# Kernel tuning notes

Hardware: AMD Instinct MI355X
Metric: run time of the kernel (lower is better)

## Reference

```python
import jax, jax.numpy as jnp
import numpy as np

B, LT, LP = 64, 128, 16   # batch, tweet len, topic len
V, H, H2 = 18000, 768, 768


def setup_inputs() -> dict:
    key = jax.random.key(0)
    ks = jax.random.split(key, 16)
    s = 1.0 / np.sqrt(H2)
    u = lambda k, shape, sc: jax.random.uniform(k, shape, jnp.float32, -sc, sc)
    return {
        "tweet": jax.random.randint(ks[0], (B, LT), 0, V, dtype=jnp.int32),
        "topic": jax.random.randint(ks[1], (B, LP), 0, V, dtype=jnp.int32),
        "beta": jnp.ones((LP,), jnp.float32) / LP,
        "emb": jax.random.normal(ks[2], (V, H), jnp.float32),
        "Wih_f": u(ks[3], (3 * H2, H), s), "Whh_f": u(ks[4], (3 * H2, H2), s),
        "bih_f": u(ks[5], (3 * H2,), s), "bhh_f": u(ks[6], (3 * H2,), s),
        "Wih_b": u(ks[7], (3 * H2, H), s), "Whh_b": u(ks[8], (3 * H2, H2), s),
        "bih_b": u(ks[9], (3 * H2,), s), "bhh_b": u(ks[10], (3 * H2,), s),
        "W_bl": u(ks[11], (2 * H2, 2 * H2), 1.0 / np.sqrt(2 * H2)),
        "det_W": u(ks[12], (2, 4 * H2), 1.0 / np.sqrt(4 * H2)),
        "det_b": u(ks[13], (2,), 1.0 / np.sqrt(4 * H2)),
    }


def _gru_dir(x, Wih, Whh, bih, bhh, reverse):
    # x: [T, N, H] (torch GRU is seq-first: axis0 is time)
    xp = jnp.einsum('tnh,gh->tng', x, Wih) + bih  # [T, N, 3*H2]
    if reverse:
        xp = xp[::-1]

    def step(h, xpt):
        g = h @ Whh.T + bhh
        xr, xz, xn = jnp.split(xpt, 3, axis=-1)
        hr, hz, hn = jnp.split(g, 3, axis=-1)
        r = jax.nn.sigmoid(xr + hr)
        z = jax.nn.sigmoid(xz + hz)
        n = jnp.tanh(xn + r * hn)
        hnew = (1.0 - z) * n + z * h
        return hnew, hnew

    h0 = jnp.zeros((x.shape[1], Whh.shape[1]), x.dtype)
    _, hs = jax.lax.scan(step, h0, xp)
    if reverse:
        hs = hs[::-1]
    return hs


def _bigru(ids, emb, Wih_f, Whh_f, bih_f, bhh_f, Wih_b, Whh_b, bih_b, bhh_b):
    x = emb[ids]  # [B, L, H]; recurrence runs over axis0 (faithful to seq-first nn.GRU)
    f = _gru_dir(x, Wih_f, Whh_f, bih_f, bhh_f, False)
    b = _gru_dir(x, Wih_b, Whh_b, bih_b, bhh_b, True)
    return jnp.concatenate([f, b], axis=-1)  # [B, L, 2*H2]


def reference(tweet, topic, beta, emb, Wih_f, Whh_f, bih_f, bhh_f,
              Wih_b, Whh_b, bih_b, bhh_b, W_bl, det_W, det_b):
    # NOTE: original uses self.gru_tweet for BOTH tweet and topic (faithful)
    tw = _bigru(tweet, emb, Wih_f, Whh_f, bih_f, bhh_f, Wih_b, Whh_b, bih_b, bhh_b)
    tp = _bigru(topic, emb, Wih_f, Whh_f, bih_f, bhh_f, Wih_b, Whh_b, bih_b, bhh_b)
    # BiLinear: S[b,t,l] = topic[b,t] @ W @ tweet[b,l]
    S = jnp.einsum('btk,kd,bld->btl', tp, W_bl, tw)
    att = jax.nn.softmax(S, axis=-1)                    # per-(b,t) softmax over tweet positions
    r = jnp.einsum('btl,bld->btd', att, tw)             # [B, LP, 2*H2]
    mean_r = jnp.einsum('btd,t->bd', r[:, :-1], beta[:-1])  # last j skipped (the `continue`)
    R = jnp.concatenate([r[:, -1], mean_r], axis=-1)    # [B, 4*H2]
    out = R @ det_W.T + det_b                           # detect logits (torch softmax call is a no-op bug)
    return out, R
```

## Files before the change

### kernel.cpp

```cpp
#include <hip/hip_runtime.h>
#include <hip/hip_bf16.h>
#include <cstdint>
#include <cstddef>

#define HD 768
#define GD 2304
#define DD 1536

typedef __attribute__((ext_vector_type(8))) short bfrag8;
typedef __attribute__((ext_vector_type(4))) float f32x4;
typedef unsigned short ushort_t;

static constexpr size_t F_XP_TWF = 0;
static constexpr size_t F_XP_TWB = 18874368;
static constexpr size_t F_XP_TPF = 37748736;
static constexpr size_t F_XP_TPB = 40108032;
static constexpr size_t F_TPWHI  = 0;
static constexpr size_t F_TPWLO  = 786432;
static constexpr size_t F_WBLT_HI = 2000000;
static constexpr size_t F_WBLT_LO = 3200000;
static constexpr size_t F_ATT    = 5000000;
static constexpr size_t F_R      = 6000000;
static constexpr size_t F_B      = 42467328;
static constexpr size_t U_XTW_HI  = 0;
static constexpr size_t U_XTW_LO  = 6291456;
static constexpr size_t U_XTP_HI  = 12582912;
static constexpr size_t U_XTP_LO  = 13369344;
static constexpr size_t U_WIHF_HI = 14155776;
static constexpr size_t U_WIHF_LO = 15925248;
static constexpr size_t U_WIHB_HI = 17694720;
static constexpr size_t U_WIHB_LO = 19464192;
static constexpr size_t U_TWHI   = 0;
static constexpr size_t U_TWLO   = 12582912;
static constexpr size_t U_TPHI   = 25165824;
static constexpr size_t U_TPLO   = 26738688;
static constexpr size_t F_WHH    = F_B + 14155776;
static constexpr size_t U_WHHF_HI = 0;
static constexpr size_t U_WHHF_LO = 1769472;
static constexpr size_t U_WHHB_HI = 3538944;
static constexpr size_t U_WHHB_LO = 5308416;
static constexpr size_t F_H      = F_WHH + 3538944;
static constexpr size_t U_HPAIR  = 442368;
static constexpr size_t U_HLO    = 221184;

__device__ __forceinline__ float sigmoidf_(float x) { return 1.f / (1.f + expf(-x)); }
__device__ __forceinline__ ushort_t f2bf(float f) {
  unsigned int u = __builtin_bit_cast(unsigned int, f);
  unsigned int r = (u + 0x7fffu + ((u >> 16) & 1u)) >> 16;
  return (ushort_t)r;
}
__device__ __forceinline__ float bf2f(ushort_t h) {
  unsigned int u = ((unsigned int)h) << 16;
  return __builtin_bit_cast(float, u);
}
__device__ __forceinline__ void glds16(const ushort_t* src, ushort_t* ldsDst) {
  __builtin_amdgcn_global_load_lds((const void*)src, (void*)ldsDst, 16, 0, 0);
}

__global__ void zero_kernel(float* __restrict__ p, int n) {
  int i = blockIdx.x * 256 + threadIdx.x;
  if (i < n) p[i] = 0.f;
}

__global__ __launch_bounds__(256) void gather_split_kernel(
    const int* __restrict__ ids, const float* __restrict__ emb,
    ushort_t* __restrict__ hi, ushort_t* __restrict__ lo, int total4)
{
  int i = blockIdx.x * 256 + threadIdx.x;
  if (i >= total4) return;
  int r = i / 192;
  int c = (i - r * 192) * 4;
  const float4 v = *reinterpret_cast<const float4*>(emb + (size_t)ids[r] * HD + c);
  float vv[4] = {v.x, v.y, v.z, v.w};
  ushort_t h[4], l[4];
#pragma unroll
  for (int e = 0; e < 4; ++e) { h[e] = f2bf(vv[e]); l[e] = f2bf(vv[e] - bf2f(h[e])); }
  size_t base = (size_t)i * 4;
  *reinterpret_cast<uint2*>(hi + base) = make_uint2((unsigned)h[0] | ((unsigned)h[1] << 16), (unsigned)h[2] | ((unsigned)h[3] << 16));
  *reinterpret_cast<uint2*>(lo + base) = make_uint2((unsigned)l[0] | ((unsigned)l[1] << 16), (unsigned)l[2] | ((unsigned)l[3] << 16));
}

__global__ __launch_bounds__(256) void split_w_kernel(
    const float* __restrict__ src, ushort_t* __restrict__ hi,
    ushort_t* __restrict__ lo, int total4)
{
  int i = blockIdx.x * 256 + threadIdx.x;
  if (i >= total4) return;
  const float4 v = *reinterpret_cast<const float4*>(src + (size_t)i * 4);
  float vv[4] = {v.x, v.y, v.z, v.w};
  ushort_t h[4], l[4];
#pragma unroll
  for (int e = 0; e < 4; ++e) { h[e] = f2bf(vv[e]); l[e] = f2bf(vv[e] - bf2f(h[e])); }
  size_t base = (size_t)i * 4;
  *reinterpret_cast<uint2*>(hi + base) = make_uint2((unsigned)h[0] | ((unsigned)h[1] << 16), (unsigned)h[2] | ((unsigned)h[3] << 16));
  *reinterpret_cast<uint2*>(lo + base) = make_uint2((unsigned)l[0] | ((unsigned)l[1] << 16), (unsigned)l[2] | ((unsigned)l[3] << 16));
}

__global__ __launch_bounds__(256) void transp_split_kernel(
    const float* __restrict__ src, ushort_t* __restrict__ hi, ushort_t* __restrict__ lo)
{
  __shared__ float t[32][33];
  const int bx = blockIdx.x, by = blockIdx.y, tid = threadIdx.x;
  const int r = tid >> 3, c4 = (tid & 7) * 4;
  const float4 v = *reinterpret_cast<const float4*>(src + (size_t)(by * 32 + r) * DD + bx * 32 + c4);
  t[r][c4 + 0] = v.x; t[r][c4 + 1] = v.y; t[r][c4 + 2] = v.z; t[r][c4 + 3] = v.w;
  __syncthreads();
  ushort_t h[4], l[4];
#pragma unroll
  for (int j = 0; j < 4; ++j) {
    float o = t[c4 + j][r];
    h[j] = f2bf(o); l[j] = f2bf(o - bf2f(h[j]));
  }
  size_t ob = (size_t)(bx * 32 + r) * DD + by * 32 + c4;
  *reinterpret_cast<uint2*>(hi + ob) = make_uint2((unsigned)h[0] | ((unsigned)h[1] << 16), (unsigned)h[2] | ((unsigned)h[3] << 16));
  *reinterpret_cast<uint2*>(lo + ob) = make_uint2((unsigned)l[0] | ((unsigned)l[1] << 16), (unsigned)l[2] | ((unsigned)l[3] << 16));
}

template<bool SPLIT_OUT>
__global__ __launch_bounds__(256, 3) void mfma_gemm_kernel(
    const ushort_t* __restrict__ Ahi, const ushort_t* __restrict__ Alo,
    const ushort_t* __restrict__ Bhi, const ushort_t* __restrict__ Blo,
    const float* __restrict__ bias, float* __restrict__ outF,
    ushort_t* __restrict__ outHi, ushort_t* __restrict__ outLo,
    const int K, const int N, const int mgc)
{
  __shared__ __align__(16) ushort_t sm[6][4096];
  const int b = blockIdx.x, nb = gridDim.x;
  const int id = (b & 7) * (nb >> 3) + (b >> 3);
  const int cg = id / mgc, mg = id % mgc;
  const size_t mBase = (size_t)mg * 128, nBase = (size_t)cg * 128;
  const int tid = threadIdx.x, lane = tid & 63, w = tid >> 6;
  const int wr = w >> 1, wc = w & 1;
  const int KB = K >> 5;

  const ushort_t* Ah = Ahi + mBase * K;
  const ushort_t* Al = Alo + mBase * K;
  const ushort_t* Bh = Bhi + nBase * K;
  const ushort_t* Bl = Blo + nBase * K;

  f32x4 acc[4][4];
#pragma unroll
  for (int i = 0; i < 4; ++i)
#pragma unroll
    for (int j = 0; j < 4; ++j) acc[i][j] = (f32x4){0.f, 0.f, 0.f, 0.f};

  auto stageF = [&](int buf, int koff) {
    ushort_t* Bt  = sm[buf * 3 + 0];
    ushort_t* At0 = sm[buf * 3 + 1];
    ushort_t* At1 = sm[buf * 3 + 2];
#pragma unroll
    for (int ii = 0; ii < 2; ++ii) {
      int i16 = w * 2 + ii;
      int row = i16 * 16 + (lane >> 2), c16 = lane & 3;
      size_t so = (size_t)row * K + (size_t)(koff + ((c16 ^ (row & 3)) << 3));
      glds16(Bh + so, Bt + i16 * 512);
      glds16(Ah + so, At0 + i16 * 512);
      glds16(Al + so, At1 + i16 * 512);
    }
  };
  auto stageP = [&](int buf, int koff) {
    ushort_t* Bt  = sm[buf * 3 + 0];
    ushort_t* At0 = sm[buf * 3 + 1];
#pragma unroll
    for (int ii = 0; ii < 2; ++ii) {
      int i16 = w * 2 + ii;
      int row = i16 * 16 + (lane >> 2), c16 = lane & 3;
      size_t so = (size_t)row * K + (size_t)(koff + ((c16 ^ (row & 3)) << 3));
      glds16(Bl + so, Bt + i16 * 512);
      glds16(Ah + so, At0 + i16 * 512);
    }
  };
  const int kch = (lane >> 4) << 4;

  auto compute = [&](int buf, bool both) {
    const char* Bt  = reinterpret_cast<const char*>(sm[buf * 3 + 0]);
    const char* At0 = reinterpret_cast<const char*>(sm[buf * 3 + 1]);
    const char* At1 = reinterpret_cast<const char*>(sm[buf * 3 + 2]);
    bfrag8 bF[4], aF[4];
#pragma unroll
    for (int j = 0; j < 4; ++j) {
      int row = wc * 64 + j * 16 + (lane & 15);
      bF[j] = *reinterpret_cast<const bfrag8*>(Bt + row * 64 + (kch ^ ((row & 3) << 4)));
    }
#pragma unroll
    for (int i = 0; i < 4; ++i) {
      int row = wr * 64 + i * 16 + (lane & 15);
      aF[i] = *reinterpret_cast<const bfrag8*>(At0 + row * 64 + (kch ^ ((row & 3) << 4)));
    }
#pragma unroll
    for (int i = 0; i < 4; ++i)
#pragma unroll
      for (int j = 0; j < 4; ++j)
        acc[i][j] = __builtin_amdgcn_mfma_f32_16x16x32_bf16(aF[i], bF[j], acc[i][j], 0, 0, 0);
    if (both) {
#pragma unroll
      for (int i = 0; i < 4; ++i) {
        int row = wr * 64 + i * 16 + (lane & 15);
        aF[i] = *reinterpret_cast<const bfrag8*>(At1 + row * 64 + (kch ^ ((row & 3) << 4)));
      }
#pragma unroll
      for (int i = 0; i < 4; ++i)
#pragma unroll
        for (int j = 0; j < 4; ++j)
          acc[i][j] = __builtin_amdgcn_mfma_f32_16x16x32_bf16(aF[i], bF[j], acc[i][j], 0, 0, 0);
    }
  };

  stageF(0, 0);
  __syncthreads();
  for (int kb = 0; kb < KB; ++kb) {
    if (kb < KB - 1) stageF((kb + 1) & 1, (kb + 1) * 32);
    else             stageP(0, 0);
    compute(kb & 1, true);
    __syncthreads();
  }
  for (int kb = 0; kb < KB; ++kb) {
    if (kb < KB - 1) stageP((kb + 1) & 1, (kb + 1) * 32);
    compute(kb & 1, false);
    __syncthreads();
  }

#pragma unroll
  for (int i = 0; i < 4; ++i)
#pragma unroll
    for (int j = 0; j < 4; ++j) {
      int col = (int)nBase + wc * 64 + j * 16 + (lane & 15);
#pragma unroll
      for (int p = 0; p < 4; ++p) {
        size_t row = mBase + wr * 64 + i * 16 + ((lane >> 4) << 2) + p;
        if constexpr (SPLIT_OUT) {
          float v = acc[i][j][p];
          ushort_t hh = f2bf(v);
          outHi[row * N + col] = hh;
          outLo[row * N + col] = f2bf(v - bf2f(hh));
        } else {
          outF[row * N + col] = acc[i][j][p] + bias[col];
        }
      }
    }
}

__global__ __launch_bounds__(256) void gru3_kernel(
    const ushort_t* __restrict__ WfHi, const ushort_t* __restrict__ WfLo,
    const ushort_t* __restrict__ WbHi, const ushort_t* __restrict__ WbLo,
    const float* __restrict__ bhhF, const float* __restrict__ bhhB,
    const float* __restrict__ xpTwf, const float* __restrict__ xpTwb,
    const float* __restrict__ xpTpf, const float* __restrict__ xpTpb,
    const ushort_t* __restrict__ Hc, ushort_t* __restrict__ Hn,
    ushort_t* __restrict__ TWhi, ushort_t* __restrict__ TWlo,
    ushort_t* __restrict__ TPhi, ushort_t* __restrict__ TPlo, const int s)
{
  __shared__ __align__(16) ushort_t sm[2][16][512];
  const int bid = blockIdx.x;
  const int xcd = bid & 7, kk = bid >> 3;
  const bool isTweet = (kk < 24);
  const int sl = isTweet ? (kk >> 2) : (kk - 24);
  const int rg = isTweet ? (kk & 3) : 0;
  const int slice = xcd * 6 + sl;
  const int cg = slice >> 1, dir = slice & 1;
  const int j0 = cg * 32;
  const int Mfrags = isTweet ? 2 : 1;
  const int baseR = dir * 144 + (isTweet ? rg * 32 : 128);
  const ushort_t* __restrict__ Whi = dir ? WbHi : WfHi;
  const ushort_t* __restrict__ Wlo = dir ? WbLo : WfLo;
  const float* __restrict__ bhh = dir ? bhhB : bhhF;
  const int tid = threadIdx.x, lane = tid & 63, w = tid >> 6;
  const ushort_t* HcHi = Hc;
  const ushort_t* HcLo = Hc + U_HLO;

  const int mf = isTweet ? (w & 1) : 0;
  const int ch = isTweet ? (w >> 1) : w;
  const bool doCompute = isTweet || (w < 2);

  auto stage = [&](int buf, int kb) {
    const int r16 = lane & 15, k8 = (lane >> 4) << 3;
#pragma unroll
    for (int i = 0; i < 4; ++i) {
      const int slot = w * 4 + i;
      if (slot < 4) {
        const int m = slot >> 1, p = slot & 1;
        if (m < Mfrags) {
          const ushort_t* src = (p ? HcLo : HcHi) +
              (size_t)(baseR + m * 16 + r16) * HD + kb * 32 + k8;
          glds16(src, &sm[buf][slot][0]);
        }
      } else {
        const int idx = slot - 4;
        const int p = idx & 1, c2 = (idx >> 1) & 1, g = idx >> 2;
        const ushort_t* W = p ? Wlo : Whi;
        const ushort_t* src = W +
            (size_t)(g * HD + j0 + c2 * 16 + r16) * HD + kb * 32 + k8;
        glds16(src, &sm[buf][slot][0]);
      }
    }
  };

  f32x4 acc[3];
#pragma unroll
  for (int g = 0; g < 3; ++g) acc[g] = (f32x4){0.f, 0.f, 0.f, 0.f};

  auto computeT = [&](int buf) {
    if (!doCompute) return;
    const char* base = reinterpret_cast<const char*>(&sm[buf][0][0]);
    const int aoff = mf * 2;
    bfrag8 Ah = *reinterpret_cast<const bfrag8*>(base + (aoff + 0) * 1024 + lane * 16);
    bfrag8 Al = *reinterpret_cast<const bfrag8*>(base + (aoff + 1) * 1024 + lane * 16);
#pragma unroll
    for (int g = 0; g < 3; ++g) {
      const int bidx = 4 + (g * 2 + ch) * 2;
      bfrag8 Bh = *reinterpret_cast<const bfrag8*>(base + (bidx + 0) * 1024 + lane * 16);
      bfrag8 Bl = *reinterpret_cast<const bfrag8*>(base + (bidx + 1) * 1024 + lane * 16);
      acc[g] = __builtin_amdgcn_mfma_f32_16x16x32_bf16(Ah, Bh, acc[g], 0, 0, 0);
      acc[g] = __builtin_amdgcn_mfma_f32_16x16x32_bf16(Al, Bh, acc[g], 0, 0, 0);
      acc[g] = __builtin_amdgcn_mfma_f32_16x16x32_bf16(Ah, Bl, acc[g], 0, 0, 0);
    }
  };

  stage(0, 0);
  __syncthreads();
  for (int kb = 0; kb < 24; ++kb) {
    if (kb < 23) stage((kb + 1) & 1, kb + 1);
    computeT(kb & 1);
    __syncthreads();
  }

  if (doCompute) {
    const int colG = j0 + ch * 16 + (lane & 15);
#pragma unroll
    for (int p = 0; p < 4; ++p) {
      const int lr = mf * 16 + ((lane >> 4) << 2) + p;
      const int gr = baseR + lr;
      const float* xp; size_t orow; int ocol; bool isTW;
      if (isTweet) {
        const int li = rg * 32 + lr;
        if (dir == 0) { xp = xpTwf + (size_t)(s * 128 + li) * GD;                 orow = (size_t)s * 128 + li;        ocol = colG;      }
        else          { const int t = 63 - s; xp = xpTwb + (size_t)(t * 128 + li) * GD; orow = (size_t)t * 128 + li;  ocol = HD + colG; }
        isTW = true;
      } else {
        const int li = lr;
        if (dir == 0) { xp = xpTpf + (size_t)(s * 16 + li) * GD;                  orow = (size_t)s * 16 + li;         ocol = colG;      }
        else          { const int t = 63 - s; xp = xpTpb + (size_t)(t * 16 + li) * GD;  orow = (size_t)t * 16 + li;   ocol = HD + colG; }
        isTW = false;
      }
      float rv = sigmoidf_(xp[colG]          + acc[0][p] + bhh[colG]);
      float zv = sigmoidf_(xp[HD + colG]     + acc[1][p] + bhh[HD + colG]);
      float nv = tanhf   (xp[2 * HD + colG]  + rv * (acc[2][p] + bhh[2 * HD + colG]));
      float hp = bf2f(HcHi[(size_t)gr * HD + colG]) + bf2f(HcLo[(size_t)gr * HD + colG]);
      float h = (1.f - zv) * nv + zv * hp;
      ushort_t hh = f2bf(h);
      ushort_t hl = f2bf(h - bf2f(hh));
      Hn[(size_t)gr * HD + colG] = hh;
      Hn[U_HLO + (size_t)gr * HD + colG] = hl;
      if (isTW) { TWhi[orow * DD + ocol] = hh; TWlo[orow * DD + ocol] = hl; }
      else      { TPhi[orow * DD + ocol] = hh; TPlo[orow * DD + ocol] = hl; }
    }
  }
}

__global__ __launch_bounds__(256) void attn_s_kernel(
    const ushort_t* __restrict__ TPWhi, const ushort_t* __restrict__ TPWlo,
    const ushort_t* __restrict__ TWhi, const ushort_t* __restrict__ TWlo,
    float* __restrict__ attg)
{
  __shared__ __align__(16) ushort_t Ah[24576];
  __shared__ __align__(16) ushort_t Al[24576];
  __shared__ __align__(16) ushort_t Bs[2][4096];
  __shared__ float Sl[16][132];
  const int b = blockIdx.x;
  const int tid = threadIdx.x, lane = tid & 63, w = tid >> 6;
  const int r = lane & 15, kc = (lane >> 4) << 3;

  {
    const ushort_t* sH = TPWhi + ((size_t)b * 16 + r) * DD + kc;
    const ushort_t* sL = TPWlo + ((size_t)b * 16 + r) * DD + kc;
#pragma unroll
    for (int ii = 0; ii < 12; ++ii) {
      int kb = w * 12 + ii;
      glds16(sH + kb * 32, Ah + kb * 512);
      glds16(sL + kb * 32, Al + kb * 512);
    }
  }
  auto stageB = [&](int buf, const ushort_t* src, int koff) {
#pragma unroll
    for (int ii = 0; ii < 2; ++ii) {
      int nf = w * 2 + ii;
      glds16(src + ((size_t)b * 128 + nf * 16 + r) * DD + koff + kc, Bs[buf] + nf * 512);
    }
  };
  stageB(0, TWhi, 0);
  __syncthreads();

  f32x4 acc[2];
  acc[0] = (f32x4){0.f, 0.f, 0.f, 0.f};
  acc[1] = (f32x4){0.f, 0.f, 0.f, 0.f};
  for (int c = 0; c < 96; ++c) {
    if (c < 95) {
      int nc = c + 1;
      stageB(nc & 1, (nc < 48) ? TWhi : TWlo, (nc % 48) * 32);
    }
    const int kb = c % 48;
    bfrag8 aH = *reinterpret_cast<const bfrag8*>(reinterpret_cast<const char*>(Ah) + kb * 1024 + lane * 16);
    bfrag8 b0 = *reinterpret_cast<const bfrag8*>(reinterpret_cast<const char*>(Bs[c & 1]) + (w * 2 + 0) * 1024 + lane * 16);
    bfrag8 b1 = *reinterpret_cast<const bfrag8*>(reinterpret_cast<const char*>(Bs[c & 1]) + (w * 2 + 1) * 1024 + lane * 16);
    acc[0] = __builtin_amdgcn_mfma_f32_16x16x32_bf16(aH, b0, acc[0], 0, 0, 0);
    acc[1] = __builtin_amdgcn_mfma_f32_16x16x32_bf16(aH, b1, acc[1], 0, 0, 0);
    if (c < 48) {
      bfrag8 aL = *reinterpret_cast<const bfrag8*>(reinterpret_cast<const char*>(Al) + kb * 1024 + lane * 16);
      acc[0] = __builtin_amdgcn_mfma_f32_16x16x32_bf16(aL, b0, acc[0], 0, 0, 0);
      acc[1] = __builtin_amdgcn_mfma_f32_16x16x32_bf16(aL, b1, acc[1], 0, 0, 0);
    }
    __syncthreads();
  }

#pragma unroll
  for (int nfl = 0; nfl < 2; ++nfl) {
    int l = (w * 2 + nfl) * 16 + (lane & 15);
#pragma unroll
    for (int p = 0; p < 4; ++p) Sl[(lane >> 4) * 4 + p][l] = acc[nfl][p];
  }
  __syncthreads();

  const int t = tid >> 4, j = tid & 15;
  float4 v0 = *reinterpret_cast<const float4*>(&Sl[t][j * 8]);
  float4 v1 = *reinterpret_cast<const float4*>(&Sl[t][j * 8 + 4]);
  float m = fmaxf(fmaxf(fmaxf(v0.x, v0.y), fmaxf(v0.z, v0.w)),
                  fmaxf(fmaxf(v1.x, v1.y), fmaxf(v1.z, v1.w)));
#pragma unroll
  for (int mk = 1; mk < 16; mk <<= 1) m = fmaxf(m, __shfl_xor(m, mk));
  float e[8];
  e[0] = expf(v0.x - m); e[1] = expf(v0.y - m); e[2] = expf(v0.z - m); e[3] = expf(v0.w - m);
  e[4] = expf(v1.x - m); e[5] = expf(v1.y - m); e[6] = expf(v1.z - m); e[7] = expf(v1.w - m);
  float ssum = e[0] + e[1] + e[2] + e[3] + e[4] + e[5] + e[6] + e[7];
#pragma unroll
  for (int mk = 1; mk < 16; mk <<= 1) ssum += __shfl_xor(ssum, mk);
  const float inv = 1.f / ssum;
  float* po = attg + (size_t)b * 2048 + t * 128 + j * 8;
  *reinterpret_cast<float4*>(po)     = make_float4(e[0] * inv, e[1] * inv, e[2] * inv, e[3] * inv);
  *reinterpret_cast<float4*>(po + 4) = make_float4(e[4] * inv, e[5] * inv, e[6] * inv, e[7] * inv);
}

__global__ __launch_bounds__(256) void r2_kernel(
    const float* __restrict__ attg, const ushort_t* __restrict__ TWhi,
    const ushort_t* __restrict__ TWlo, float* __restrict__ Rr)
{
  __shared__ float al[2048];
  const int b = blockIdx.y;
  const int d = blockIdx.x * 256 + threadIdx.x;
  for (int i = threadIdx.x; i < 2048; i += 256) al[i] = attg[(size_t)b * 2048 + i];
  __syncthreads();
  float racc[16];
#pragma unroll
  for (int t = 0; t < 16; ++t) racc[t] = 0.f;
  for (int l = 0; l < 128; ++l) {
    size_t o = ((size_t)b * 128 + l) * DD + d;
    float tw = bf2f(TWhi[o]) + bf2f(TWlo[o]);
#pragma unroll
    for (int t = 0; t < 16; ++t) racc[t] += al[t * 128 + l] * tw;
  }
#pragma unroll
  for (int t = 0; t < 16; ++t) Rr[((size_t)b * 16 + t) * DD + d] = racc[t];
}

__global__ __launch_bounds__(256) void final_kernel(
    const float* __restrict__ Rr, const float* __restrict__ beta,
    const float* __restrict__ detW, const float* __restrict__ detb,
    float* __restrict__ dout)
{
  __shared__ float bet[16];
  __shared__ float red0[256], red1[256];
  const int b = blockIdx.x, tid = threadIdx.x;
  if (tid < 16) bet[tid] = beta[tid];
  __syncthreads();
  const float* rb = Rr + (size_t)b * 16 * DD;
  float* Rout = dout + 128 + (size_t)b * 3072;
  float p0 = 0.f, p1 = 0.f;
  for (int d = tid; d < 3072; d += 256) {
    float v;
    if (d < DD) {
      v = rb[15 * DD + d];
    } else {
      float sum = 0.f;
#pragma unroll
      for (int tt = 0; tt < 15; ++tt) sum += bet[tt] * rb[(size_t)tt * DD + (d - DD)];
      v = sum;
    }
    Rout[d] = v;
    p0 += v * detW[d];
    p1 += v * detW[3072 + d];
  }
  red0[tid] = p0; red1[tid] = p1;
  __syncthreads();
  for (int off = 128; off > 0; off >>= 1) {
    if (tid < off) { red0[tid] += red0[tid + off]; red1[tid] += red1[tid + off]; }
    __syncthreads();
  }
  if (tid == 0) {
    dout[b * 2 + 0] = red0[0] + detb[0];
    dout[b * 2 + 1] = red1[0] + detb[1];
  }
}

extern "C" void kernel_launch(void* const* d_in, const int* in_sizes, int n_in,
                              void* d_out, int out_size, void* d_ws, size_t ws_size,
                              hipStream_t stream)
{
  (void)in_sizes; (void)n_in; (void)out_size; (void)ws_size;
  const int*   tweet = (const int*)  d_in[0];
  const int*   topic = (const int*)  d_in[1];
  const float* beta  = (const float*)d_in[2];
  const float* emb   = (const float*)d_in[3];
  const float* Wih_f = (const float*)d_in[4];
  const float* Whh_f = (const float*)d_in[5];
  const float* bih_f = (const float*)d_in[6];
  const float* bhh_f = (const float*)d_in[7];
  const float* Wih_b = (const float*)d_in[8];
  const float* Whh_b = (const float*)d_in[9];
  const float* bih_b = (const float*)d_in[10];
  const float* bhh_b = (const float*)d_in[11];
  const float* W_bl  = (const float*)d_in[12];
  const float* det_W = (const float*)d_in[13];
  const float* det_b = (const float*)d_in[14];

  float* ws = (float*)d_ws;
  float* xp_twf = ws + F_XP_TWF;
  float* xp_twb = ws + F_XP_TWB;
  float* xp_tpf = ws + F_XP_TPF;
  float* xp_tpb = ws + F_XP_TPB;
  float* attg   = ws + F_ATT;
  float* Rr     = ws + F_R;
  ushort_t* TPWhi = (ushort_t*)(ws + F_TPWHI);
  ushort_t* TPWlo = (ushort_t*)(ws + F_TPWLO);
  ushort_t* WblTh = (ushort_t*)(ws + F_WBLT_HI);
  ushort_t* WblTl = (ushort_t*)(ws + F_WBLT_LO);
  ushort_t* uB    = (ushort_t*)(ws + F_B);
  ushort_t* uWhh  = (ushort_t*)(ws + F_WHH);
  ushort_t* uH    = (ushort_t*)(ws + F_H);

  zero_kernel<<<dim3(864), dim3(256), 0, stream>>>(ws + F_H, 221184);

  gather_split_kernel<<<dim3(6144), dim3(256), 0, stream>>>(tweet, emb, uB + U_XTW_HI, uB + U_XTW_LO, 1572864);
  gather_split_kernel<<<dim3(768),  dim3(256), 0, stream>>>(topic, emb, uB + U_XTP_HI, uB + U_XTP_LO, 196608);
  split_w_kernel<<<dim3(1728), dim3(256), 0, stream>>>(Wih_f, uB + U_WIHF_HI, uB + U_WIHF_LO, 442368);
  split_w_kernel<<<dim3(1728), dim3(256), 0, stream>>>(Wih_b, uB + U_WIHB_HI, uB + U_WIHB_LO, 442368);
  split_w_kernel<<<dim3(1728), dim3(256), 0, stream>>>(Whh_f, uWhh + U_WHHF_HI, uWhh + U_WHHF_LO, 442368);
  split_w_kernel<<<dim3(1728), dim3(256), 0, stream>>>(Whh_b, uWhh + U_WHHB_HI, uWhh + U_WHHB_LO, 442368);

  mfma_gemm_kernel<false><<<dim3(1152), dim3(256), 0, stream>>>(uB + U_XTW_HI, uB + U_XTW_LO, uB + U_WIHF_HI, uB + U_WIHF_LO, bih_f, xp_twf, nullptr, nullptr, HD, GD, 64);
  mfma_gemm_kernel<false><<<dim3(1152), dim3(256), 0, stream>>>(uB + U_XTW_HI, uB + U_XTW_LO, uB + U_WIHB_HI, uB + U_WIHB_LO, bih_b, xp_twb, nullptr, nullptr, HD, GD, 64);
  mfma_gemm_kernel<false><<<dim3(144),  dim3(256), 0, stream>>>(uB + U_XTP_HI, uB + U_XTP_LO, uB + U_WIHF_HI, uB + U_WIHF_LO, bih_f, xp_tpf, nullptr, nullptr, HD, GD, 8);
  mfma_gemm_kernel<false><<<dim3(144),  dim3(256), 0, stream>>>(uB + U_XTP_HI, uB + U_XTP_LO, uB + U_WIHB_HI, uB + U_WIHB_LO, bih_b, xp_tpb, nullptr, nullptr, HD, GD, 8);

  for (int s = 0; s < 64; ++s) {
    const ushort_t* Hc = uH + (size_t)(s & 1) * U_HPAIR;
    ushort_t*       Hn = uH + (size_t)((s & 1) ^ 1) * U_HPAIR;
    gru3_kernel<<<dim3(240), dim3(256), 0, stream>>>(
        uWhh + U_WHHF_HI, uWhh + U_WHHF_LO, uWhh + U_WHHB_HI, uWhh + U_WHHB_LO,
        bhh_f, bhh_b, xp_twf, xp_twb, xp_tpf, xp_tpb, Hc, Hn,
        uB + U_TWHI, uB + U_TWLO, uB + U_TPHI, uB + U_TPLO, s);
  }

  transp_split_kernel<<<dim3(48, 48), dim3(256), 0, stream>>>(W_bl, WblTh, WblTl);
  mfma_gemm_kernel<true><<<dim3(96), dim3(256), 0, stream>>>(uB + U_TPHI, uB + U_TPLO, WblTh, WblTl, nullptr, nullptr, TPWhi, TPWlo, DD, DD, 8);
  attn_s_kernel<<<dim3(64), dim3(256), 0, stream>>>(TPWhi, TPWlo, uB + U_TWHI, uB + U_TWLO, attg);
  r2_kernel<<<dim3(6, 64), dim3(256), 0, stream>>>(attg, uB + U_TWHI, uB + U_TWLO, Rr);
  final_kernel<<<dim3(64), dim3(256), 0, stream>>>(Rr, beta, det_W, det_b, (float*)d_out);
}
```

Before: 1.879 ms.

## Deepen GRU step prefetch to four-stage ring and remap GEMM blocks per XCD

The recurrent GRU kernel moves from double-buffered shared memory to a four-slot ring, keeping three k-blocks of global-to-LDS loads in flight. It waits on explicit vmcnt counters before each raw s_barrier. The H loads are made unconditional so every wave issues the same number of loads and the counts stay valid. Separately, the input-projection GEMM block-to-tile mapping is changed so each XCD handles a contiguous range of M tiles, which is meant to improve L2 reuse. The ring doubles LDS use and relies on hand-set waitcnt values matching the exact load count.

```diff
diff --git a/kernel.cpp b/kernel.cpp
--- a/kernel.cpp
+++ b/kernel.cpp
@@ -125,9 +125,11 @@
     const int K, const int N, const int mgc)
 {
   __shared__ __align__(16) ushort_t sm[6][4096];
-  const int b = blockIdx.x, nb = gridDim.x;
-  const int id = (b & 7) * (nb >> 3) + (b >> 3);
-  const int cg = id / mgc, mg = id % mgc;
+  const int b = blockIdx.x;
+  const int xcdq = b & 7, off = b >> 3;
+  const int mpx = mgc >> 3;
+  const int mg = xcdq * mpx + (off % mpx);
+  const int cg = off / mpx;
   const size_t mBase = (size_t)mg * 128, nBase = (size_t)cg * 128;
   const int tid = threadIdx.x, lane = tid & 63, w = tid >> 6;
   const int wr = w >> 1, wc = w & 1;
@@ -240,7 +242,7 @@
     }
 }
 
-__global__ __launch_bounds__(256) void gru3_kernel(
+__global__ __launch_bounds__(256) void gru4_kernel(
     const ushort_t* __restrict__ WfHi, const ushort_t* __restrict__ WfLo,
     const ushort_t* __restrict__ WbHi, const ushort_t* __restrict__ WbLo,
     const float* __restrict__ bhhF, const float* __restrict__ bhhB,
@@ -250,7 +252,7 @@
     ushort_t* __restrict__ TWhi, ushort_t* __restrict__ TWlo,
     ushort_t* __restrict__ TPhi, ushort_t* __restrict__ TPlo, const int s)
 {
-  __shared__ __align__(16) ushort_t sm[2][16][512];
+  __shared__ __align__(16) ushort_t sm[4][16][512];
   const int bid = blockIdx.x;
   const int xcd = bid & 7, kk = bid >> 3;
   const bool isTweet = (kk < 24);
@@ -277,21 +279,18 @@
 #pragma unroll
     for (int i = 0; i < 4; ++i) {
       const int slot = w * 4 + i;
+      const ushort_t* src;
       if (slot < 4) {
         const int m = slot >> 1, p = slot & 1;
-        if (m < Mfrags) {
-          const ushort_t* src = (p ? HcLo : HcHi) +
-              (size_t)(baseR + m * 16 + r16) * HD + kb * 32 + k8;
-          glds16(src, &sm[buf][slot][0]);
-        }
+        const int mm = (m < Mfrags) ? m : 0;
+        src = (p ? HcLo : HcHi) + (size_t)(baseR + mm * 16 + r16) * HD + kb * 32 + k8;
       } else {
         const int idx = slot - 4;
         const int p = idx & 1, c2 = (idx >> 1) & 1, g = idx >> 2;
         const ushort_t* W = p ? Wlo : Whi;
-        const ushort_t* src = W +
-            (size_t)(g * HD + j0 + c2 * 16 + r16) * HD + kb * 32 + k8;
-        glds16(src, &sm[buf][slot][0]);
+        src = W + (size_t)(g * HD + j0 + c2 * 16 + r16) * HD + kb * 32 + k8;
       }
+      glds16(src, &sm[buf][slot][0]);
     }
   };
 
@@ -316,12 +315,16 @@
     }
   };
 
-  stage(0, 0);
-  __syncthreads();
+  stage(0, 0); stage(1, 1); stage(2, 2);
+#pragma unroll
   for (int kb = 0; kb < 24; ++kb) {
-    if (kb < 23) stage((kb + 1) & 1, kb + 1);
-    computeT(kb & 1);
-    __syncthreads();
+    if (kb < 22)       asm volatile("s_waitcnt vmcnt(8)" ::: "memory");
+    else if (kb == 22) asm volatile("s_waitcnt vmcnt(4)" ::: "memory");
+    else               asm volatile("s_waitcnt vmcnt(0)" ::: "memory");
+    __builtin_amdgcn_s_barrier();
+    __builtin_amdgcn_sched_barrier(0);
+    computeT(kb & 3);
+    if (kb < 21) stage((kb + 3) & 3, kb + 3);
   }
 
   if (doCompute) {
@@ -553,7 +556,7 @@
   for (int s = 0; s < 64; ++s) {
     const ushort_t* Hc = uH + (size_t)(s & 1) * U_HPAIR;
     ushort_t*       Hn = uH + (size_t)((s & 1) ^ 1) * U_HPAIR;
-    gru3_kernel<<<dim3(240), dim3(256), 0, stream>>>(
+    gru4_kernel<<<dim3(240), dim3(256), 0, stream>>>(
         uWhh + U_WHHF_HI, uWhh + U_WHHF_LO, uWhh + U_WHHB_HI, uWhh + U_WHHB_LO,
         bhh_f, bhh_b, xp_twf, xp_twb, xp_tpf, xp_tpb, Hc, Hn,
         uB + U_TWHI, uB + U_TWLO, uB + U_TPHI, uB + U_TPLO, s);
```

Result: faster. 1.609 ms (-14.4%).
